# Kernel optimization log

Hardware: AMD Instinct MI355X
Metric: run time of the kernel (lower is better)

## Reference

```python
import jax, jax.numpy as jnp
import numpy as np

B, K, D, A = 32768, 16, 256, 64
SCALE = A ** -0.5


def setup_inputs() -> dict:
    key = jax.random.key(0)
    ks = jax.random.split(key, 10)
    s = 1.0 / np.sqrt(D)
    s2 = 1.0 / np.sqrt(2 * D)
    return {
        "center_emb": jax.random.normal(ks[0], (B, D), jnp.float32),
        "neigh_embs": jax.random.normal(ks[1], (B, K, D), jnp.float32),
        "neigh_weights": jax.random.uniform(ks[2], (B, K), jnp.float32),
        "valid_mask": jax.random.randint(ks[3], (B,), 0, 2) > 0,
        "Wq": jax.random.uniform(ks[4], (A, D), jnp.float32, -s, s),
        "bq": jnp.zeros((A,), jnp.float32),
        "Wk": jax.random.uniform(ks[5], (A, D), jnp.float32, -s, s),
        "bk": jnp.zeros((A,), jnp.float32),
        "Wg": jax.random.uniform(ks[6], (D, 2 * D), jnp.float32, -s2, s2),
        "bg": jnp.zeros((D,), jnp.float32),
    }


def reference(center_emb, neigh_embs, neigh_weights, valid_mask, Wq, bq, Wk, bk, Wg, bg):
    # q: [B, A]; k: [B, K, A]
    q = center_emb @ Wq.T + bq
    k = jnp.einsum("bkd,ad->bka", neigh_embs, Wk) + bk
    # scaled dot-product attention over K neighbors
    attn = jax.nn.softmax(jnp.einsum("ba,bka->bk", q, k) * SCALE, axis=-1)
    # confidence reweighting + renormalize
    attn = attn * neigh_weights
    attn = attn / (attn.sum(axis=-1, keepdims=True) + 1e-8)
    # dropout is identity in eval mode
    context = jnp.einsum("bk,bkd->bd", attn, neigh_embs)  # [B, D]
    gate_in = jnp.concatenate([center_emb, context], axis=-1)  # [B, 2D]
    gate = jax.nn.sigmoid(gate_in @ Wg.T + bg)
    fused = gate * center_emb + (1.0 - gate) * context
    return jnp.where(valid_mask[:, None], fused, center_emb)
```

## Files before the change

### kernel.cpp

```cpp
#include <hip/hip_runtime.h>
#include <hip/hip_bf16.h>

#define DDIM   256
#define KNBR   16
#define TWOD   512
#define NTHREADS 256

using bf16x8  = __attribute__((ext_vector_type(8))) short;
using short4v = __attribute__((ext_vector_type(4))) short;
using f32x4   = __attribute__((ext_vector_type(4))) float;

#define CTX_SOFF 163840u
#define QG_BOFF  17104896u
#define WS_NEED  25493504u

__device__ __forceinline__ short f2bf(float x) {
  unsigned int u;
  __builtin_memcpy(&u, &x, 4);
  u += 0x7FFFu + ((u >> 16) & 1u);
  return (short)(u >> 16);
}
__device__ __forceinline__ float bf2f(short s) {
  unsigned int u = ((unsigned int)(unsigned short)s) << 16;
  float f;
  __builtin_memcpy(&f, &u, 4);
  return f;
}

__device__ __forceinline__ bf16x8 ldWfrag(const float* __restrict__ W, int ld, int r, int c) {
  const float4* p = (const float4*)(W + (size_t)r * ld + c);
  float4 a = p[0];
  float4 b = p[1];
  bf16x8 o;
  o[0] = f2bf(a.x); o[1] = f2bf(a.y); o[2] = f2bf(a.z); o[3] = f2bf(a.w);
  o[4] = f2bf(b.x); o[5] = f2bf(b.y); o[6] = f2bf(b.z); o[7] = f2bf(b.w);
  return o;
}

__global__ void prep_frags(const float* __restrict__ Wq,
                           const float* __restrict__ Wk,
                           const float* __restrict__ Wg,
                           short* __restrict__ F) {
  const int gid  = blockIdx.x * NTHREADS + threadIdx.x;
  const int lane = gid & 63;
  const int n16  = lane & 15;
  const int g4   = lane >> 4;
  const int f    = gid >> 6;
  const float* src;
  short* dst;
  if (f < 32) {
    const int t = f >> 3, s = f & 7;
    src = Wq + (size_t)(t * 16 + n16) * DDIM + s * 32 + g4 * 8;
    dst = F + f * 512 + lane * 8;
  } else if (f < 64) {
    const int fq = f - 32;
    const int t = fq >> 3, s = fq & 7;
    src = Wk + (size_t)(t * 16 + n16) * DDIM + s * 32 + g4 * 8;
    dst = F + 16384 + fq * 512 + lane * 8;
  } else {
    const int fg = f - 64;
    const int t4 = fg >> 4, s = fg & 15;
    src = Wg + (size_t)(t4 * 16 + n16) * TWOD + s * 32 + g4 * 8;
    dst = F + 32768 + fg * 512 + lane * 8;
  }
  float4 a = *(const float4*)src;
  float4 b = *(const float4*)(src + 4);
  bf16x8 o;
  o[0] = f2bf(a.x); o[1] = f2bf(a.y); o[2] = f2bf(a.z); o[3] = f2bf(a.w);
  o[4] = f2bf(b.x); o[5] = f2bf(b.y); o[6] = f2bf(b.z); o[7] = f2bf(b.w);
  *(bf16x8*)dst = o;
}

__global__ __launch_bounds__(NTHREADS, 4)
void k_q(const float* __restrict__ center, const short* __restrict__ WF,
         const float* __restrict__ bq, float* __restrict__ qg) {
  __shared__ __align__(16) short sCen[4096];
  const int tid  = threadIdx.x;
  const int lane = tid & 63;
  const int w    = tid >> 6;
  const int n16  = lane & 15;
  const int g4   = lane >> 4;
  const int row0 = blockIdx.x * 16;
  const short* WqF = WF;

  #pragma unroll
  for (int it = 0; it < 4; ++it) {
    const int row = it * 4 + w;
    const int d   = lane * 4;
    float4 v = *(const float4*)(center + (size_t)(row0 + row) * DDIM + d);
    short4v o;
    o[0] = f2bf(v.x); o[1] = f2bf(v.y); o[2] = f2bf(v.z); o[3] = f2bf(v.w);
    *(short4v*)&sCen[(row * 256 + d) ^ ((row & 7) << 3)] = o;
  }
  __syncthreads();

  f32x4 qacc;
  qacc[0]=0.f; qacc[1]=0.f; qacc[2]=0.f; qacc[3]=0.f;
  #pragma unroll
  for (int s = 0; s < 8; ++s) {
    bf16x8 af = *(const bf16x8*)&sCen[(n16 * 256 + s * 32 + g4 * 8) ^ ((n16 & 7) << 3)];
    bf16x8 bfr = *(const bf16x8*)&WqF[(w * 8 + s) * 512 + lane * 8];
    qacc = __builtin_amdgcn_mfma_f32_16x16x32_bf16(af, bfr, qacc, 0, 0, 0);
  }
  const float bqa = bq[w * 16 + n16];
  #pragma unroll
  for (int r = 0; r < 4; ++r) {
    const size_t row = (size_t)(row0 + g4 * 4 + r);
    qg[row * 64 + w * 16 + n16] = qacc[r] + bqa;
  }
}

__global__ __launch_bounds__(NTHREADS, 4)
void natt_ctx2(const float* __restrict__ neigh, const float* __restrict__ nwts,
               const float* __restrict__ qg, const short* __restrict__ WF,
               const float* __restrict__ bk, short* __restrict__ ctxg) {
  __shared__ __align__(16) short sNbr[16384];
  const int tid  = threadIdx.x;
  const int lane = tid & 63;
  const int w    = tid >> 6;
  const int n16  = lane & 15;
  const int g4   = lane >> 4;
  const size_t gr = (size_t)blockIdx.x * 4 + w;
  const short* WkF = WF + 16384;

  const float4* np = (const float4*)(neigh + gr * (size_t)(KNBR * DDIM));
  float4 nb0 = np[0*64+lane], nb1 = np[1*64+lane], nb2 = np[2*64+lane], nb3 = np[3*64+lane];
  float4 nb4 = np[4*64+lane], nb5 = np[5*64+lane], nb6 = np[6*64+lane], nb7 = np[7*64+lane];
  float4 nb8 = np[8*64+lane], nb9 = np[9*64+lane], nbA = np[10*64+lane], nbB = np[11*64+lane];
  float4 nbC = np[12*64+lane], nbD = np[13*64+lane], nbE = np[14*64+lane], nbF = np[15*64+lane];
  f32x4 w0 = *(const f32x4*)(nwts + gr * KNBR + 0);
  f32x4 w1 = *(const f32x4*)(nwts + gr * KNBR + 4);
  f32x4 w2 = *(const f32x4*)(nwts + gr * KNBR + 8);
  f32x4 w3 = *(const f32x4*)(nwts + gr * KNBR + 12);
  f32x4 qvv, bkv;
  #pragma unroll
  for (int t = 0; t < 4; ++t) {
    qvv[t] = qg[gr * 64 + t * 16 + n16];
    bkv[t] = bk[t * 16 + n16];
  }

  #define STG(j, v) { short4v o_;                                                   \
    o_[0]=f2bf((v).x); o_[1]=f2bf((v).y); o_[2]=f2bf((v).z); o_[3]=f2bf((v).w);     \
    *(short4v*)&sNbr[w * 4096 + (((j) * 256 + lane * 4) ^ (((j) & 7) << 3))] = o_; }
  STG(0,nb0)  STG(1,nb1)  STG(2,nb2)  STG(3,nb3)
  STG(4,nb4)  STG(5,nb5)  STG(6,nb6)  STG(7,nb7)
  STG(8,nb8)  STG(9,nb9)  STG(10,nbA) STG(11,nbB)
  STG(12,nbC) STG(13,nbD) STG(14,nbE) STG(15,nbF)
  #undef STG

  f32x4 kacc[4];
  #pragma unroll
  for (int t = 0; t < 4; ++t) { kacc[t][0]=0.f; kacc[t][1]=0.f; kacc[t][2]=0.f; kacc[t][3]=0.f; }
  #pragma unroll
  for (int s = 0; s < 8; ++s) {
    bf16x8 af = *(const bf16x8*)&sNbr[w * 4096 +
                  ((n16 * 256 + s * 32 + g4 * 8) ^ ((n16 & 7) << 3))];
    #pragma unroll
    for (int t = 0; t < 4; ++t) {
      bf16x8 bfr = *(const bf16x8*)&WkF[(t * 8 + s) * 512 + lane * 8];
      kacc[t] = __builtin_amdgcn_mfma_f32_16x16x32_bf16(af, bfr, kacc[t], 0, 0, 0);
    }
  }

  f32x4 part;
  part[0]=0.f; part[1]=0.f; part[2]=0.f; part[3]=0.f;
  #pragma unroll
  for (int t = 0; t < 4; ++t) {
    #pragma unroll
    for (int r = 0; r < 4; ++r) part[r] += qvv[t] * (kacc[t][r] + bkv[t]);
  }
  #pragma unroll
  for (int off = 1; off < 16; off <<= 1) {
    #pragma unroll
    for (int r = 0; r < 4; ++r) part[r] += __shfl_xor(part[r], off);
  }
  f32x4 lg[4];
  #pragma unroll
  for (int j = 0; j < 16; ++j)
    lg[j >> 2][j & 3] = 0.125f * __shfl(part[j & 3], (j >> 2) << 4);
  float mx = -1e30f;
  #pragma unroll
  for (int j = 0; j < 16; ++j) mx = fmaxf(mx, lg[j >> 2][j & 3]);
  float sum = 0.f;
  #pragma unroll
  for (int j = 0; j < 16; ++j) {
    const float e = __expf(lg[j >> 2][j & 3] - mx);
    lg[j >> 2][j & 3] = e; sum += e;
  }
  const float rs = 1.f / sum;
  float den = 1e-8f;
  #pragma unroll
  for (int e = 0; e < 4; ++e) {
    lg[0][e] *= rs * w0[e]; den += lg[0][e];
    lg[1][e] *= rs * w1[e]; den += lg[1][e];
    lg[2][e] *= rs * w2[e]; den += lg[2][e];
    lg[3][e] *= rs * w3[e]; den += lg[3][e];
  }
  const float rd = 1.f / den;

  f32x4 cx;
  cx[0]=0.f; cx[1]=0.f; cx[2]=0.f; cx[3]=0.f;
  #pragma unroll
  for (int j = 0; j < 16; ++j) {
    short4v nv = *(const short4v*)&sNbr[w * 4096 + ((j * 256 + lane * 4) ^ ((j & 7) << 3))];
    const float aj = lg[j >> 2][j & 3];
    cx[0] += aj * bf2f(nv[0]); cx[1] += aj * bf2f(nv[1]);
    cx[2] += aj * bf2f(nv[2]); cx[3] += aj * bf2f(nv[3]);
  }
  short4v co;
  co[0] = f2bf(cx[0] * rd); co[1] = f2bf(cx[1] * rd);
  co[2] = f2bf(cx[2] * rd); co[3] = f2bf(cx[3] * rd);
  *(short4v*)(ctxg + gr * DDIM + lane * 4) = co;
}

__global__ __launch_bounds__(NTHREADS, 4)
void natt_gate(const float* __restrict__ center, const short* __restrict__ ctxg,
               const void* __restrict__ vmask, const short* __restrict__ WF,
               const float* __restrict__ bg, float* __restrict__ out) {
  __shared__ __align__(16) short sCen[4096];
  __shared__ __align__(16) short sCtx[4096];
  const int tid  = threadIdx.x;
  const int lane = tid & 63;
  const int w    = tid >> 6;
  const int n16  = lane & 15;
  const int g4   = lane >> 4;
  const int row0 = blockIdx.x * 16;
  const unsigned char* mb = (const unsigned char*)vmask;
  const short* WgF = WF + 32768;

  const unsigned char x1 = mb[lane * 4 + 1];
  const unsigned char x2 = mb[lane * 4 + 2];
  const unsigned char x3 = mb[lane * 4 + 3];
  const bool anyGe2 = __ballot((x1 >= 2) || (x2 >= 2) || (x3 >= 2)) != 0ULL;
  const bool anyNz  = __ballot(((x1 | x2) | x3) != 0) != 0ULL;
  const bool maskIsByte = anyNz && !anyGe2;

  #pragma unroll
  for (int it = 0; it < 4; ++it) {
    const int row = it * 4 + w;
    const int d   = lane * 4;
    float4 v = *(const float4*)(center + (size_t)(row0 + row) * DDIM + d);
    short4v o;
    o[0] = f2bf(v.x); o[1] = f2bf(v.y); o[2] = f2bf(v.z); o[3] = f2bf(v.w);
    *(short4v*)&sCen[(row * 256 + d) ^ ((row & 7) << 3)] = o;
    short4v cv = *(const short4v*)(ctxg + (size_t)(row0 + row) * DDIM + d);
    *(short4v*)&sCtx[(row * 256 + d) ^ ((row & 7) << 3)] = cv;
  }
  __syncthreads();

  f32x4 gacc[4];
  #pragma unroll
  for (int t = 0; t < 4; ++t) { gacc[t][0]=0.f; gacc[t][1]=0.f; gacc[t][2]=0.f; gacc[t][3]=0.f; }
  #pragma unroll
  for (int s = 0; s < 16; ++s) {
    bf16x8 af;
    if (s < 8) {
      af = *(const bf16x8*)&sCen[(n16 * 256 + s * 32 + g4 * 8) ^ ((n16 & 7) << 3)];
    } else {
      af = *(const bf16x8*)&sCtx[(n16 * 256 + (s - 8) * 32 + g4 * 8) ^ ((n16 & 7) << 3)];
    }
    #pragma unroll
    for (int tt = 0; tt < 4; ++tt) {
      bf16x8 bfr = *(const bf16x8*)&WgF[((w * 4 + tt) * 16 + s) * 512 + lane * 8];
      gacc[tt] = __builtin_amdgcn_mfma_f32_16x16x32_bf16(af, bfr, gacc[tt], 0, 0, 0);
    }
  }
  #pragma unroll
  for (int tt = 0; tt < 4; ++tt) {
    const int dout = (w * 4 + tt) * 16 + n16;
    const float bga = bg[dout];
    #pragma unroll
    for (int r = 0; r < 4; ++r) {
      const int rowl = g4 * 4 + r;
      const size_t gr = (size_t)(row0 + rowl);
      const float pre  = gacc[tt][r] + bga;
      const float gate = 1.f / (1.f + __expf(-pre));
      const float cen  = center[gr * DDIM + dout];
      const float cxv  = bf2f(sCtx[(rowl * 256 + dout) ^ ((rowl & 7) << 3)]);
      const float fused = gate * cen + (1.f - gate) * cxv;
      const bool valid = maskIsByte ? (mb[gr] != 0)
                                    : (((const unsigned int*)vmask)[gr] != 0u);
      out[gr * DDIM + dout] = valid ? fused : cen;
    }
  }
}

__global__ __launch_bounds__(NTHREADS, 3)
void natt_fb(const float* __restrict__ center, const float* __restrict__ neigh,
             const float* __restrict__ nwts, const void* __restrict__ vmask,
             const float* __restrict__ Wq, const float* __restrict__ bq,
             const float* __restrict__ Wk, const float* __restrict__ bk,
             const float* __restrict__ Wg, const float* __restrict__ bg,
             float* __restrict__ out) {
  __shared__ __align__(16) short smem[24576];
  const int tid  = threadIdx.x;
  const int lane = tid & 63;
  const int w    = tid >> 6;
  const int n16  = lane & 15;
  const int g4   = lane >> 4;
  const int row0 = blockIdx.x * 16;
  const unsigned char* mb = (const unsigned char*)vmask;

  const unsigned char x1 = mb[lane * 4 + 1];
  const unsigned char x2 = mb[lane * 4 + 2];
  const unsigned char x3 = mb[lane * 4 + 3];
  const bool anyGe2 = __ballot((x1 >= 2) || (x2 >= 2) || (x3 >= 2)) != 0ULL;
  const bool anyNz  = __ballot(((x1 | x2) | x3) != 0) != 0ULL;
  const bool maskIsByte = anyNz && !anyGe2;

  #pragma unroll
  for (int it = 0; it < 4; ++it) {
    const int row = it * 4 + w;
    const int d   = lane * 4;
    float4 v = *(const float4*)(center + (size_t)(row0 + row) * DDIM + d);
    short4v o;
    o[0] = f2bf(v.x); o[1] = f2bf(v.y); o[2] = f2bf(v.z); o[3] = f2bf(v.w);
    *(short4v*)&smem[16384 + ((row * 512 + d) ^ ((row & 7) << 3))] = o;
  }
  __syncthreads();

  f32x4 qacc[4];
  #pragma unroll
  for (int t = 0; t < 4; ++t) { qacc[t][0]=0.f; qacc[t][1]=0.f; qacc[t][2]=0.f; qacc[t][3]=0.f; }
  #pragma unroll
  for (int s = 0; s < 8; ++s) {
    bf16x8 af = *(const bf16x8*)&smem[16384 + ((n16 * 512 + s * 32 + g4 * 8) ^ ((n16 & 7) << 3))];
    #pragma unroll
    for (int t = 0; t < 4; ++t) {
      bf16x8 bfr = ldWfrag(Wq, DDIM, t * 16 + n16, s * 32 + g4 * 8);
      qacc[t] = __builtin_amdgcn_mfma_f32_16x16x32_bf16(af, bfr, qacc[t], 0, 0, 0);
    }
  }
  f32x4 bqv, bkv;
  #pragma unroll
  for (int t = 0; t < 4; ++t) { bqv[t] = bq[t * 16 + n16]; bkv[t] = bk[t * 16 + n16]; }

  for (int rr = 0; rr < 4; ++rr) {
    const int rowl = w * 4 + rr;
    const size_t gr = (size_t)(row0 + rowl);
    const float4* np = (const float4*)(neigh + gr * (size_t)(KNBR * DDIM));
    {
      float4 vb[8];
      #pragma unroll
      for (int j = 0; j < 8; ++j) vb[j] = np[j * 64 + lane];
      #pragma unroll
      for (int j = 0; j < 8; ++j) {
        short4v o;
        o[0]=f2bf(vb[j].x); o[1]=f2bf(vb[j].y); o[2]=f2bf(vb[j].z); o[3]=f2bf(vb[j].w);
        *(short4v*)&smem[w * 4096 + ((j * 256 + lane * 4) ^ ((j & 7) << 3))] = o;
      }
      #pragma unroll
      for (int j = 0; j < 8; ++j) vb[j] = np[(j + 8) * 64 + lane];
      #pragma unroll
      for (int j = 0; j < 8; ++j) {
        short4v o;
        o[0]=f2bf(vb[j].x); o[1]=f2bf(vb[j].y); o[2]=f2bf(vb[j].z); o[3]=f2bf(vb[j].w);
        *(short4v*)&smem[w * 4096 + (((j + 8) * 256 + lane * 4) ^ (((j + 8) & 7) << 3))] = o;
      }
    }
    f32x4 kacc[4];
    #pragma unroll
    for (int t = 0; t < 4; ++t) { kacc[t][0]=0.f; kacc[t][1]=0.f; kacc[t][2]=0.f; kacc[t][3]=0.f; }
    #pragma unroll
    for (int s = 0; s < 8; ++s) {
      bf16x8 af = *(const bf16x8*)&smem[w * 4096 +
                    ((n16 * 256 + s * 32 + g4 * 8) ^ ((n16 & 7) << 3))];
      #pragma unroll
      for (int t = 0; t < 4; ++t) {
        bf16x8 bfr = ldWfrag(Wk, DDIM, t * 16 + n16, s * 32 + g4 * 8);
        kacc[t] = __builtin_amdgcn_mfma_f32_16x16x32_bf16(af, bfr, kacc[t], 0, 0, 0);
      }
    }
    f32x4 part;
    part[0]=0.f; part[1]=0.f; part[2]=0.f; part[3]=0.f;
    #pragma unroll
    for (int t = 0; t < 4; ++t) {
      float qv = qacc[t][0];
      if (rr == 1) qv = qacc[t][1];
      if (rr == 2) qv = qacc[t][2];
      if (rr == 3) qv = qacc[t][3];
      qv = __shfl(qv + bqv[t], w * 16 + n16);
      #pragma unroll
      for (int r = 0; r < 4; ++r) part[r] += qv * (kacc[t][r] + bkv[t]);
    }
    #pragma unroll
    for (int off = 1; off < 16; off <<= 1) {
      #pragma unroll
      for (int r = 0; r < 4; ++r) part[r] += __shfl_xor(part[r], off);
    }
    f32x4 lg[4];
    #pragma unroll
    for (int j = 0; j < 16; ++j)
      lg[j >> 2][j & 3] = 0.125f * __shfl(part[j & 3], (j >> 2) << 4);
    float mx = -1e30f;
    #pragma unroll
    for (int j = 0; j < 16; ++j) mx = fmaxf(mx, lg[j >> 2][j & 3]);
    float sum = 0.f;
    #pragma unroll
    for (int j = 0; j < 16; ++j) {
      const float e = __expf(lg[j >> 2][j & 3] - mx);
      lg[j >> 2][j & 3] = e; sum += e;
    }
    const float rs = 1.f / sum;
    float den = 1e-8f;
    #pragma unroll
    for (int q4 = 0; q4 < 4; ++q4) {
      f32x4 wvq = *(const f32x4*)(nwts + gr * KNBR + q4 * 4);
      #pragma unroll
      for (int e = 0; e < 4; ++e) { const float a = lg[q4][e] * rs * wvq[e]; lg[q4][e] = a; den += a; }
    }
    const float rd = 1.f / den;
    f32x4 cx;
    cx[0]=0.f; cx[1]=0.f; cx[2]=0.f; cx[3]=0.f;
    #pragma unroll
    for (int j = 0; j < 16; ++j) {
      short4v nv = *(const short4v*)&smem[w * 4096 + ((j * 256 + lane * 4) ^ ((j & 7) << 3))];
      const float aj = lg[j >> 2][j & 3];
      cx[0] += aj * bf2f(nv[0]); cx[1] += aj * bf2f(nv[1]);
      cx[2] += aj * bf2f(nv[2]); cx[3] += aj * bf2f(nv[3]);
    }
    short4v co;
    co[0] = f2bf(cx[0] * rd); co[1] = f2bf(cx[1] * rd);
    co[2] = f2bf(cx[2] * rd); co[3] = f2bf(cx[3] * rd);
    *(short4v*)&smem[16384 + ((rowl * 512 + 256 + lane * 4) ^ ((rowl & 7) << 3))] = co;
  }
  __syncthreads();

  f32x4 gacc[4];
  #pragma unroll
  for (int t = 0; t < 4; ++t) { gacc[t][0]=0.f; gacc[t][1]=0.f; gacc[t][2]=0.f; gacc[t][3]=0.f; }
  #pragma unroll
  for (int s = 0; s < 16; ++s) {
    bf16x8 af = *(const bf16x8*)&smem[16384 + ((n16 * 512 + s * 32 + g4 * 8) ^ ((n16 & 7) << 3))];
    #pragma unroll
    for (int tt = 0; tt < 4; ++tt) {
      bf16x8 bfr = ldWfrag(Wg, TWOD, (w * 4 + tt) * 16 + n16, s * 32 + g4 * 8);
      gacc[tt] = __builtin_amdgcn_mfma_f32_16x16x32_bf16(af, bfr, gacc[tt], 0, 0, 0);
    }
  }
  #pragma unroll
  for (int tt = 0; tt < 4; ++tt) {
    const int dout = (w * 4 + tt) * 16 + n16;
    const float bga = bg[dout];
    #pragma unroll
    for (int r = 0; r < 4; ++r) {
      const int rowl = g4 * 4 + r;
      const size_t gr = (size_t)(row0 + rowl);
      const float pre  = gacc[tt][r] + bga;
      const float gate = 1.f / (1.f + __expf(-pre));
      const float cen  = center[gr * DDIM + dout];
      const float cxv  = bf2f(smem[16384 + ((rowl * 512 + 256 + dout) ^ ((rowl & 7) << 3))]);
      const float fused = gate * cen + (1.f - gate) * cxv;
      const bool valid = maskIsByte ? (mb[gr] != 0)
                                    : (((const unsigned int*)vmask)[gr] != 0u);
      out[gr * DDIM + dout] = valid ? fused : cen;
    }
  }
}

extern "C" void kernel_launch(void* const* d_in, const int* in_sizes, int n_in,
                              void* d_out, int out_size, void* d_ws, size_t ws_size,
                              hipStream_t stream) {
  const float* center = (const float*)d_in[0];
  const float* neigh  = (const float*)d_in[1];
  const float* nwts   = (const float*)d_in[2];
  const void*  vm     = d_in[3];
  const float* Wq = (const float*)d_in[4];
  const float* bq = (const float*)d_in[5];
  const float* Wk = (const float*)d_in[6];
  const float* bk = (const float*)d_in[7];
  const float* Wg = (const float*)d_in[8];
  const float* bg = (const float*)d_in[9];
  float* out = (float*)d_out;

  const int nrows = in_sizes[0] / DDIM;
  dim3 block(NTHREADS);

  if (ws_size >= (size_t)WS_NEED) {
    short* WF   = (short*)d_ws;
    short* ctxg = WF + CTX_SOFF;
    float* qg   = (float*)((char*)d_ws + QG_BOFF);
    hipLaunchKernelGGL(prep_frags, dim3(80), block, 0, stream, Wq, Wk, Wg, WF);
    hipLaunchKernelGGL(k_q, dim3(nrows / 16), block, 0, stream, center, WF, bq, qg);
    hipLaunchKernelGGL(natt_ctx2, dim3(nrows / 4), block, 0, stream,
                       neigh, nwts, qg, WF, bk, ctxg);
    hipLaunchKernelGGL(natt_gate, dim3(nrows / 16), block, 0, stream,
                       center, ctxg, vm, WF, bg, out);
  } else {
    hipLaunchKernelGGL(natt_fb, dim3(nrows / 16), block, 0, stream,
                       center, neigh, nwts, vm, Wq, bq, Wk, bk, Wg, bg, out);
  }
}
```

Baseline: 178.5 us.

## Load neighbor tiles directly into LDS as fp32 via global_load_lds

Replaces register-staged loading of neighbor embeddings (load to VGPRs, convert to bf16, store to LDS) with direct global-to-LDS DMA loads of fp32 data, using an XOR swizzle on the source address. The bf16 conversion moves to the MFMA operand read, and the context sum now uses the fp32 values. The goal is to cut register pressure and VALU conversion work on the memory-bound main kernel. In exchange, LDS per block doubles to 64KB and launch bounds drop to 2 blocks per CU, which lowers occupancy and latency hiding.

```diff
diff --git a/kernel.cpp b/kernel.cpp
--- a/kernel.cpp
+++ b/kernel.cpp
@@ -110,11 +110,11 @@
   }
 }
 
-__global__ __launch_bounds__(NTHREADS, 4)
-void natt_ctx2(const float* __restrict__ neigh, const float* __restrict__ nwts,
+__global__ __launch_bounds__(NTHREADS, 2)
+void natt_ctx3(const float* __restrict__ neigh, const float* __restrict__ nwts,
                const float* __restrict__ qg, const short* __restrict__ WF,
                const float* __restrict__ bk, short* __restrict__ ctxg) {
-  __shared__ __align__(16) short sNbr[16384];
+  __shared__ __align__(16) float sNbrF[16384];
   const int tid  = threadIdx.x;
   const int lane = tid & 63;
   const int w    = tid >> 6;
@@ -123,11 +123,15 @@
   const size_t gr = (size_t)blockIdx.x * 4 + w;
   const short* WkF = WF + 16384;
 
-  const float4* np = (const float4*)(neigh + gr * (size_t)(KNBR * DDIM));
-  float4 nb0 = np[0*64+lane], nb1 = np[1*64+lane], nb2 = np[2*64+lane], nb3 = np[3*64+lane];
-  float4 nb4 = np[4*64+lane], nb5 = np[5*64+lane], nb6 = np[6*64+lane], nb7 = np[7*64+lane];
-  float4 nb8 = np[8*64+lane], nb9 = np[9*64+lane], nbA = np[10*64+lane], nbB = np[11*64+lane];
-  float4 nbC = np[12*64+lane], nbD = np[13*64+lane], nbE = np[14*64+lane], nbF = np[15*64+lane];
+  const float* nbase = neigh + gr * (size_t)(KNBR * DDIM);
+  #pragma unroll
+  for (int j = 0; j < 16; ++j) {
+    const float* gsrc = nbase + j * 256 + ((lane * 4) ^ ((j & 7) << 2));
+    float* ldst = &sNbrF[w * 4096 + j * 256];
+    __builtin_amdgcn_global_load_lds((const __attribute__((address_space(1))) void*)gsrc,
+                                     (__attribute__((address_space(3))) void*)ldst,
+                                     16, 0, 0);
+  }
   f32x4 w0 = *(const f32x4*)(nwts + gr * KNBR + 0);
   f32x4 w1 = *(const f32x4*)(nwts + gr * KNBR + 4);
   f32x4 w2 = *(const f32x4*)(nwts + gr * KNBR + 8);
@@ -138,23 +142,20 @@
     qvv[t] = qg[gr * 64 + t * 16 + n16];
     bkv[t] = bk[t * 16 + n16];
   }
-
-  #define STG(j, v) { short4v o_;                                                   \
-    o_[0]=f2bf((v).x); o_[1]=f2bf((v).y); o_[2]=f2bf((v).z); o_[3]=f2bf((v).w);     \
-    *(short4v*)&sNbr[w * 4096 + (((j) * 256 + lane * 4) ^ (((j) & 7) << 3))] = o_; }
-  STG(0,nb0)  STG(1,nb1)  STG(2,nb2)  STG(3,nb3)
-  STG(4,nb4)  STG(5,nb5)  STG(6,nb6)  STG(7,nb7)
-  STG(8,nb8)  STG(9,nb9)  STG(10,nbA) STG(11,nbB)
-  STG(12,nbC) STG(13,nbD) STG(14,nbE) STG(15,nbF)
-  #undef STG
+  asm volatile("s_waitcnt vmcnt(0)" ::: "memory");
 
   f32x4 kacc[4];
   #pragma unroll
   for (int t = 0; t < 4; ++t) { kacc[t][0]=0.f; kacc[t][1]=0.f; kacc[t][2]=0.f; kacc[t][3]=0.f; }
+  const int xr = (n16 & 7) << 2;
   #pragma unroll
   for (int s = 0; s < 8; ++s) {
-    bf16x8 af = *(const bf16x8*)&sNbr[w * 4096 +
-                  ((n16 * 256 + s * 32 + g4 * 8) ^ ((n16 & 7) << 3))];
+    const int c0 = s * 32 + g4 * 8;
+    f32x4 a0 = *(const f32x4*)&sNbrF[w * 4096 + n16 * 256 + (c0 ^ xr)];
+    f32x4 a1 = *(const f32x4*)&sNbrF[w * 4096 + n16 * 256 + ((c0 + 4) ^ xr)];
+    bf16x8 af;
+    af[0]=f2bf(a0[0]); af[1]=f2bf(a0[1]); af[2]=f2bf(a0[2]); af[3]=f2bf(a0[3]);
+    af[4]=f2bf(a1[0]); af[5]=f2bf(a1[1]); af[6]=f2bf(a1[2]); af[7]=f2bf(a1[3]);
     #pragma unroll
     for (int t = 0; t < 4; ++t) {
       bf16x8 bfr = *(const bf16x8*)&WkF[(t * 8 + s) * 512 + lane * 8];
@@ -202,10 +203,10 @@
   cx[0]=0.f; cx[1]=0.f; cx[2]=0.f; cx[3]=0.f;
   #pragma unroll
   for (int j = 0; j < 16; ++j) {
-    short4v nv = *(const short4v*)&sNbr[w * 4096 + ((j * 256 + lane * 4) ^ ((j & 7) << 3))];
+    f32x4 nv = *(const f32x4*)&sNbrF[w * 4096 + j * 256 + ((lane * 4) ^ ((j & 7) << 2))];
     const float aj = lg[j >> 2][j & 3];
-    cx[0] += aj * bf2f(nv[0]); cx[1] += aj * bf2f(nv[1]);
-    cx[2] += aj * bf2f(nv[2]); cx[3] += aj * bf2f(nv[3]);
+    cx[0] += aj * nv[0]; cx[1] += aj * nv[1];
+    cx[2] += aj * nv[2]; cx[3] += aj * nv[3];
   }
   short4v co;
   co[0] = f2bf(cx[0] * rd); co[1] = f2bf(cx[1] * rd);
@@ -482,7 +483,7 @@
     float* qg   = (float*)((char*)d_ws + QG_BOFF);
     hipLaunchKernelGGL(prep_frags, dim3(80), block, 0, stream, Wq, Wk, Wg, WF);
     hipLaunchKernelGGL(k_q, dim3(nrows / 16), block, 0, stream, center, WF, bq, qg);
-    hipLaunchKernelGGL(natt_ctx2, dim3(nrows / 4), block, 0, stream,
+    hipLaunchKernelGGL(natt_ctx3, dim3(nrows / 4), block, 0, stream,
                        neigh, nwts, qg, WF, bk, ctxg);
     hipLaunchKernelGGL(natt_gate, dim3(nrows / 16), block, 0, stream,
                        center, ctxg, vm, WF, bg, out);
```

After: 188.1 us. +5.4%, slower.

## Fuse query projection into neighbor-attention kernel and drop separate q launch

Applied to the files above, without the earlier changes.

Removes the standalone k_q kernel and computes the query projection inside the context kernel. Each wave projects its own center row using MFMA with the row broadcast across all 16 A-rows. This removes one launch and the global write and read of the q buffer, and shrinks the workspace. In exchange it spends extra MFMA work, since 16x redundant rows are computed and only the first is used. It also uses more registers and LDS, and launch bounds drop from 4 to 3 waves-per-EU occupancy.

```diff
diff --git a/kernel.cpp b/kernel.cpp
--- a/kernel.cpp
+++ b/kernel.cpp
@@ -11,8 +11,7 @@
 using f32x4   = __attribute__((ext_vector_type(4))) float;
 
 #define CTX_SOFF 163840u
-#define QG_BOFF  17104896u
-#define WS_NEED  25493504u
+#define WS_NEED  17104896u
 
 __device__ __forceinline__ short f2bf(float x) {
   unsigned int u;
@@ -71,56 +70,20 @@
   *(bf16x8*)dst = o;
 }
 
-__global__ __launch_bounds__(NTHREADS, 4)
-void k_q(const float* __restrict__ center, const short* __restrict__ WF,
-         const float* __restrict__ bq, float* __restrict__ qg) {
-  __shared__ __align__(16) short sCen[4096];
-  const int tid  = threadIdx.x;
-  const int lane = tid & 63;
-  const int w    = tid >> 6;
-  const int n16  = lane & 15;
-  const int g4   = lane >> 4;
-  const int row0 = blockIdx.x * 16;
-  const short* WqF = WF;
-
-  #pragma unroll
-  for (int it = 0; it < 4; ++it) {
-    const int row = it * 4 + w;
-    const int d   = lane * 4;
-    float4 v = *(const float4*)(center + (size_t)(row0 + row) * DDIM + d);
-    short4v o;
-    o[0] = f2bf(v.x); o[1] = f2bf(v.y); o[2] = f2bf(v.z); o[3] = f2bf(v.w);
-    *(short4v*)&sCen[(row * 256 + d) ^ ((row & 7) << 3)] = o;
-  }
-  __syncthreads();
-
-  f32x4 qacc;
-  qacc[0]=0.f; qacc[1]=0.f; qacc[2]=0.f; qacc[3]=0.f;
-  #pragma unroll
-  for (int s = 0; s < 8; ++s) {
-    bf16x8 af = *(const bf16x8*)&sCen[(n16 * 256 + s * 32 + g4 * 8) ^ ((n16 & 7) << 3)];
-    bf16x8 bfr = *(const bf16x8*)&WqF[(w * 8 + s) * 512 + lane * 8];
-    qacc = __builtin_amdgcn_mfma_f32_16x16x32_bf16(af, bfr, qacc, 0, 0, 0);
-  }
-  const float bqa = bq[w * 16 + n16];
-  #pragma unroll
-  for (int r = 0; r < 4; ++r) {
-    const size_t row = (size_t)(row0 + g4 * 4 + r);
-    qg[row * 64 + w * 16 + n16] = qacc[r] + bqa;
-  }
-}
-
-__global__ __launch_bounds__(NTHREADS, 4)
-void natt_ctx2(const float* __restrict__ neigh, const float* __restrict__ nwts,
-               const float* __restrict__ qg, const short* __restrict__ WF,
-               const float* __restrict__ bk, short* __restrict__ ctxg) {
+__global__ __launch_bounds__(NTHREADS, 3)
+void natt_ctx2p(const float* __restrict__ center, const float* __restrict__ neigh,
+                const float* __restrict__ nwts, const short* __restrict__ WF,
+                const float* __restrict__ bq, const float* __restrict__ bk,
+                short* __restrict__ ctxg) {
   __shared__ __align__(16) short sNbr[16384];
+  __shared__ __align__(16) short sCen[1024];
   const int tid  = threadIdx.x;
   const int lane = tid & 63;
   const int w    = tid >> 6;
   const int n16  = lane & 15;
   const int g4   = lane >> 4;
   const size_t gr = (size_t)blockIdx.x * 4 + w;
+  const short* WqF = WF;
   const short* WkF = WF + 16384;
 
   const float4* np = (const float4*)(neigh + gr * (size_t)(KNBR * DDIM));
@@ -128,16 +91,36 @@
   float4 nb4 = np[4*64+lane], nb5 = np[5*64+lane], nb6 = np[6*64+lane], nb7 = np[7*64+lane];
   float4 nb8 = np[8*64+lane], nb9 = np[9*64+lane], nbA = np[10*64+lane], nbB = np[11*64+lane];
   float4 nbC = np[12*64+lane], nbD = np[13*64+lane], nbE = np[14*64+lane], nbF = np[15*64+lane];
+
+  {
+    float4 cv = *(const float4*)(center + gr * DDIM + lane * 4);
+    short4v o;
+    o[0] = f2bf(cv.x); o[1] = f2bf(cv.y); o[2] = f2bf(cv.z); o[3] = f2bf(cv.w);
+    *(short4v*)&sCen[(w * 256 + lane * 4) ^ (w << 3)] = o;
+  }
+
+  f32x4 qacc[4];
+  #pragma unroll
+  for (int t = 0; t < 4; ++t) { qacc[t][0]=0.f; qacc[t][1]=0.f; qacc[t][2]=0.f; qacc[t][3]=0.f; }
+  #pragma unroll
+  for (int s = 0; s < 8; ++s) {
+    bf16x8 af = *(const bf16x8*)&sCen[(w * 256 + s * 32 + g4 * 8) ^ (w << 3)];
+    #pragma unroll
+    for (int t = 0; t < 4; ++t) {
+      bf16x8 bfr = *(const bf16x8*)&WqF[(t * 8 + s) * 512 + lane * 8];
+      qacc[t] = __builtin_amdgcn_mfma_f32_16x16x32_bf16(af, bfr, qacc[t], 0, 0, 0);
+    }
+  }
+  f32x4 qvv, bkv;
+  #pragma unroll
+  for (int t = 0; t < 4; ++t) {
+    qvv[t] = qacc[t][0] + bq[t * 16 + n16];
+    bkv[t] = bk[t * 16 + n16];
+  }
   f32x4 w0 = *(const f32x4*)(nwts + gr * KNBR + 0);
   f32x4 w1 = *(const f32x4*)(nwts + gr * KNBR + 4);
   f32x4 w2 = *(const f32x4*)(nwts + gr * KNBR + 8);
   f32x4 w3 = *(const f32x4*)(nwts + gr * KNBR + 12);
-  f32x4 qvv, bkv;
-  #pragma unroll
-  for (int t = 0; t < 4; ++t) {
-    qvv[t] = qg[gr * 64 + t * 16 + n16];
-    bkv[t] = bk[t * 16 + n16];
-  }
 
   #define STG(j, v) { short4v o_;                                                   \
     o_[0]=f2bf((v).x); o_[1]=f2bf((v).y); o_[2]=f2bf((v).z); o_[3]=f2bf((v).w);     \
@@ -479,11 +462,9 @@
   if (ws_size >= (size_t)WS_NEED) {
     short* WF   = (short*)d_ws;
     short* ctxg = WF + CTX_SOFF;
-    float* qg   = (float*)((char*)d_ws + QG_BOFF);
     hipLaunchKernelGGL(prep_frags, dim3(80), block, 0, stream, Wq, Wk, Wg, WF);
-    hipLaunchKernelGGL(k_q, dim3(nrows / 16), block, 0, stream, center, WF, bq, qg);
-    hipLaunchKernelGGL(natt_ctx2, dim3(nrows / 4), block, 0, stream,
-                       neigh, nwts, qg, WF, bk, ctxg);
+    hipLaunchKernelGGL(natt_ctx2p, dim3(nrows / 4), block, 0, stream,
+                       center, neigh, nwts, WF, bq, bk, ctxg);
     hipLaunchKernelGGL(natt_gate, dim3(nrows / 16), block, 0, stream,
                        center, ctxg, vm, WF, bg, out);
   } else {
```

New measurement: 184.9 us. 3.6% more time.

## Process two rows per wave, prefetching the second row during the first

Applied to the files above, without the earlier changes.

The context kernel now gives each wave two neighbor rows instead of one, and launches half as many blocks. The second row's global loads are issued into registers before the first row's MFMA, softmax and context work runs, so memory latency overlaps with compute. The per-row compute moves into a shared inline helper. The cost is higher register pressure, with launch bounds relaxed from 4 to 3 blocks per CU, which may lower occupancy in a kernel that is mostly bandwidth-bound.

```diff
diff --git a/kernel.cpp b/kernel.cpp
--- a/kernel.cpp
+++ b/kernel.cpp
@@ -110,8 +110,86 @@
   }
 }
 
-__global__ __launch_bounds__(NTHREADS, 4)
-void natt_ctx2(const float* __restrict__ neigh, const float* __restrict__ nwts,
+__device__ __forceinline__ void row_compute(
+    int w, int lane, int n16, int g4, size_t gr,
+    const float* __restrict__ nwts, const float* __restrict__ qg,
+    const short* __restrict__ WkF, const f32x4& bkv,
+    const short* __restrict__ sNbr, short* __restrict__ ctxg) {
+  f32x4 qvv;
+  #pragma unroll
+  for (int t = 0; t < 4; ++t) qvv[t] = qg[gr * 64 + t * 16 + n16];
+  f32x4 w0 = *(const f32x4*)(nwts + gr * KNBR + 0);
+  f32x4 w1 = *(const f32x4*)(nwts + gr * KNBR + 4);
+  f32x4 w2 = *(const f32x4*)(nwts + gr * KNBR + 8);
+  f32x4 w3 = *(const f32x4*)(nwts + gr * KNBR + 12);
+
+  f32x4 kacc[4];
+  #pragma unroll
+  for (int t = 0; t < 4; ++t) { kacc[t][0]=0.f; kacc[t][1]=0.f; kacc[t][2]=0.f; kacc[t][3]=0.f; }
+  #pragma unroll
+  for (int s = 0; s < 8; ++s) {
+    bf16x8 af = *(const bf16x8*)&sNbr[w * 4096 +
+                  ((n16 * 256 + s * 32 + g4 * 8) ^ ((n16 & 7) << 3))];
+    #pragma unroll
+    for (int t = 0; t < 4; ++t) {
+      bf16x8 bfr = *(const bf16x8*)&WkF[(t * 8 + s) * 512 + lane * 8];
+      kacc[t] = __builtin_amdgcn_mfma_f32_16x16x32_bf16(af, bfr, kacc[t], 0, 0, 0);
+    }
+  }
+
+  f32x4 part;
+  part[0]=0.f; part[1]=0.f; part[2]=0.f; part[3]=0.f;
+  #pragma unroll
+  for (int t = 0; t < 4; ++t) {
+    #pragma unroll
+    for (int r = 0; r < 4; ++r) part[r] += qvv[t] * (kacc[t][r] + bkv[t]);
+  }
+  #pragma unroll
+  for (int off = 1; off < 16; off <<= 1) {
+    #pragma unroll
+    for (int r = 0; r < 4; ++r) part[r] += __shfl_xor(part[r], off);
+  }
+  f32x4 lg[4];
+  #pragma unroll
+  for (int j = 0; j < 16; ++j)
+    lg[j >> 2][j & 3] = 0.125f * __shfl(part[j & 3], (j >> 2) << 4);
+  float mx = -1e30f;
+  #pragma unroll
+  for (int j = 0; j < 16; ++j) mx = fmaxf(mx, lg[j >> 2][j & 3]);
+  float sum = 0.f;
+  #pragma unroll
+  for (int j = 0; j < 16; ++j) {
+    const float e = __expf(lg[j >> 2][j & 3] - mx);
+    lg[j >> 2][j & 3] = e; sum += e;
+  }
+  const float rs = 1.f / sum;
+  float den = 1e-8f;
+  #pragma unroll
+  for (int e = 0; e < 4; ++e) {
+    lg[0][e] *= rs * w0[e]; den += lg[0][e];
+    lg[1][e] *= rs * w1[e]; den += lg[1][e];
+    lg[2][e] *= rs * w2[e]; den += lg[2][e];
+    lg[3][e] *= rs * w3[e]; den += lg[3][e];
+  }
+  const float rd = 1.f / den;
+
+  f32x4 cx;
+  cx[0]=0.f; cx[1]=0.f; cx[2]=0.f; cx[3]=0.f;
+  #pragma unroll
+  for (int j = 0; j < 16; ++j) {
+    short4v nv = *(const short4v*)&sNbr[w * 4096 + ((j * 256 + lane * 4) ^ ((j & 7) << 3))];
+    const float aj = lg[j >> 2][j & 3];
+    cx[0] += aj * bf2f(nv[0]); cx[1] += aj * bf2f(nv[1]);
+    cx[2] += aj * bf2f(nv[2]); cx[3] += aj * bf2f(nv[3]);
+  }
+  short4v co;
+  co[0] = f2bf(cx[0] * rd); co[1] = f2bf(cx[1] * rd);
+  co[2] = f2bf(cx[2] * rd); co[3] = f2bf(cx[3] * rd);
+  *(short4v*)(ctxg + gr * DDIM + lane * 4) = co;
+}
+
+__global__ __launch_bounds__(NTHREADS, 3)
+void natt_ctx5(const float* __restrict__ neigh, const float* __restrict__ nwts,
                const float* __restrict__ qg, const short* __restrict__ WF,
                const float* __restrict__ bk, short* __restrict__ ctxg) {
   __shared__ __align__(16) short sNbr[16384];
@@ -120,97 +198,43 @@
   const int w    = tid >> 6;
   const int n16  = lane & 15;
   const int g4   = lane >> 4;
-  const size_t gr = (size_t)blockIdx.x * 4 + w;
+  const size_t gr0 = (size_t)blockIdx.x * 8 + w;
+  const size_t gr1 = gr0 + 4;
   const short* WkF = WF + 16384;
-
-  const float4* np = (const float4*)(neigh + gr * (size_t)(KNBR * DDIM));
-  float4 nb0 = np[0*64+lane], nb1 = np[1*64+lane], nb2 = np[2*64+lane], nb3 = np[3*64+lane];
-  float4 nb4 = np[4*64+lane], nb5 = np[5*64+lane], nb6 = np[6*64+lane], nb7 = np[7*64+lane];
-  float4 nb8 = np[8*64+lane], nb9 = np[9*64+lane], nbA = np[10*64+lane], nbB = np[11*64+lane];
-  float4 nbC = np[12*64+lane], nbD = np[13*64+lane], nbE = np[14*64+lane], nbF = np[15*64+lane];
-  f32x4 w0 = *(const f32x4*)(nwts + gr * KNBR + 0);
-  f32x4 w1 = *(const f32x4*)(nwts + gr * KNBR + 4);
-  f32x4 w2 = *(const f32x4*)(nwts + gr * KNBR + 8);
-  f32x4 w3 = *(const f32x4*)(nwts + gr * KNBR + 12);
-  f32x4 qvv, bkv;
-  #pragma unroll
-  for (int t = 0; t < 4; ++t) {
-    qvv[t] = qg[gr * 64 + t * 16 + n16];
-    bkv[t] = bk[t * 16 + n16];
-  }
+  f32x4 bkv;
+  #pragma unroll
+  for (int t = 0; t < 4; ++t) bkv[t] = bk[t * 16 + n16];
+
+  const float4* np0 = (const float4*)(neigh + gr0 * (size_t)(KNBR * DDIM));
+  float4 nb0 = np0[0*64+lane], nb1 = np0[1*64+lane], nb2 = np0[2*64+lane], nb3 = np0[3*64+lane];
+  float4 nb4 = np0[4*64+lane], nb5 = np0[5*64+lane], nb6 = np0[6*64+lane], nb7 = np0[7*64+lane];
+  float4 nb8 = np0[8*64+lane], nb9 = np0[9*64+lane], nbA = np0[10*64+lane], nbB = np0[11*64+lane];
+  float4 nbC = np0[12*64+lane], nbD = np0[13*64+lane], nbE = np0[14*64+lane], nbF = np0[15*64+lane];
 
   #define STG(j, v) { short4v o_;                                                   \
     o_[0]=f2bf((v).x); o_[1]=f2bf((v).y); o_[2]=f2bf((v).z); o_[3]=f2bf((v).w);     \
     *(short4v*)&sNbr[w * 4096 + (((j) * 256 + lane * 4) ^ (((j) & 7) << 3))] = o_; }
+
+  STG(0,nb0)  STG(1,nb1)  STG(2,nb2)  STG(3,nb3)
+  STG(4,nb4)  STG(5,nb5)  STG(6,nb6)  STG(7,nb7)
+  STG(8,nb8)  STG(9,nb9)  STG(10,nbA) STG(11,nbB)
+  STG(12,nbC) STG(13,nbD) STG(14,nbE) STG(15,nbF)
+
+  const float4* np1 = (const float4*)(neigh + gr1 * (size_t)(KNBR * DDIM));
+  nb0 = np1[0*64+lane];  nb1 = np1[1*64+lane];  nb2 = np1[2*64+lane];  nb3 = np1[3*64+lane];
+  nb4 = np1[4*64+lane];  nb5 = np1[5*64+lane];  nb6 = np1[6*64+lane];  nb7 = np1[7*64+lane];
+  nb8 = np1[8*64+lane];  nb9 = np1[9*64+lane];  nbA = np1[10*64+lane]; nbB = np1[11*64+lane];
+  nbC = np1[12*64+lane]; nbD = np1[13*64+lane]; nbE = np1[14*64+lane]; nbF = np1[15*64+lane];
+
+  row_compute(w, lane, n16, g4, gr0, nwts, qg, WkF, bkv, sNbr, ctxg);
+
   STG(0,nb0)  STG(1,nb1)  STG(2,nb2)  STG(3,nb3)
   STG(4,nb4)  STG(5,nb5)  STG(6,nb6)  STG(7,nb7)
   STG(8,nb8)  STG(9,nb9)  STG(10,nbA) STG(11,nbB)
   STG(12,nbC) STG(13,nbD) STG(14,nbE) STG(15,nbF)
   #undef STG
 
-  f32x4 kacc[4];
-  #pragma unroll
-  for (int t = 0; t < 4; ++t) { kacc[t][0]=0.f; kacc[t][1]=0.f; kacc[t][2]=0.f; kacc[t][3]=0.f; }
-  #pragma unroll
-  for (int s = 0; s < 8; ++s) {
-    bf16x8 af = *(const bf16x8*)&sNbr[w * 4096 +
-                  ((n16 * 256 + s * 32 + g4 * 8) ^ ((n16 & 7) << 3))];
-    #pragma unroll
-    for (int t = 0; t < 4; ++t) {
-      bf16x8 bfr = *(const bf16x8*)&WkF[(t * 8 + s) * 512 + lane * 8];
-      kacc[t] = __builtin_amdgcn_mfma_f32_16x16x32_bf16(af, bfr, kacc[t], 0, 0, 0);
-    }
-  }
-
-  f32x4 part;
-  part[0]=0.f; part[1]=0.f; part[2]=0.f; part[3]=0.f;
-  #pragma unroll
-  for (int t = 0; t < 4; ++t) {
-    #pragma unroll
-    for (int r = 0; r < 4; ++r) part[r] += qvv[t] * (kacc[t][r] + bkv[t]);
-  }
-  #pragma unroll
-  for (int off = 1; off < 16; off <<= 1) {
-    #pragma unroll
-    for (int r = 0; r < 4; ++r) part[r] += __shfl_xor(part[r], off);
-  }
-  f32x4 lg[4];
-  #pragma unroll
-  for (int j = 0; j < 16; ++j)
-    lg[j >> 2][j & 3] = 0.125f * __shfl(part[j & 3], (j >> 2) << 4);
-  float mx = -1e30f;
-  #pragma unroll
-  for (int j = 0; j < 16; ++j) mx = fmaxf(mx, lg[j >> 2][j & 3]);
-  float sum = 0.f;
-  #pragma unroll
-  for (int j = 0; j < 16; ++j) {
-    const float e = __expf(lg[j >> 2][j & 3] - mx);
-    lg[j >> 2][j & 3] = e; sum += e;
-  }
-  const float rs = 1.f / sum;
-  float den = 1e-8f;
-  #pragma unroll
-  for (int e = 0; e < 4; ++e) {
-    lg[0][e] *= rs * w0[e]; den += lg[0][e];
-    lg[1][e] *= rs * w1[e]; den += lg[1][e];
-    lg[2][e] *= rs * w2[e]; den += lg[2][e];
-    lg[3][e] *= rs * w3[e]; den += lg[3][e];
-  }
-  const float rd = 1.f / den;
-
-  f32x4 cx;
-  cx[0]=0.f; cx[1]=0.f; cx[2]=0.f; cx[3]=0.f;
-  #pragma unroll
-  for (int j = 0; j < 16; ++j) {
-    short4v nv = *(const short4v*)&sNbr[w * 4096 + ((j * 256 + lane * 4) ^ ((j & 7) << 3))];
-    const float aj = lg[j >> 2][j & 3];
-    cx[0] += aj * bf2f(nv[0]); cx[1] += aj * bf2f(nv[1]);
-    cx[2] += aj * bf2f(nv[2]); cx[3] += aj * bf2f(nv[3]);
-  }
-  short4v co;
-  co[0] = f2bf(cx[0] * rd); co[1] = f2bf(cx[1] * rd);
-  co[2] = f2bf(cx[2] * rd); co[3] = f2bf(cx[3] * rd);
-  *(short4v*)(ctxg + gr * DDIM + lane * 4) = co;
+  row_compute(w, lane, n16, g4, gr1, nwts, qg, WkF, bkv, sNbr, ctxg);
 }
 
 __global__ __launch_bounds__(NTHREADS, 4)
@@ -482,7 +506,7 @@
     float* qg   = (float*)((char*)d_ws + QG_BOFF);
     hipLaunchKernelGGL(prep_frags, dim3(80), block, 0, stream, Wq, Wk, Wg, WF);
     hipLaunchKernelGGL(k_q, dim3(nrows / 16), block, 0, stream, center, WF, bq, qg);
-    hipLaunchKernelGGL(natt_ctx2, dim3(nrows / 4), block, 0, stream,
+    hipLaunchKernelGGL(natt_ctx5, dim3(nrows / 8), block, 0, stream,
                        neigh, nwts, qg, WF, bk, ctxg);
     hipLaunchKernelGGL(natt_gate, dim3(nrows / 16), block, 0, stream,
                        center, ctxg, vm, WF, bg, out);
```

Result: slower. 241.5 us (+35.3%).
